# Kernel optimization log

Hardware: AMD Instinct MI355X
Metric: run time of the kernel (lower is better)

## Reference

```python
import jax, jax.numpy as jnp
import numpy as np

N_NODES = 50000
N_EDGES = 800000
L, D_IN, D_HID, D_OUT = 3, 128, 256, 128


def setup_inputs() -> dict:
    key = jax.random.key(0)
    ks = jax.random.split(key, 5)
    x = jax.random.normal(ks[0], (N_NODES, D_IN), dtype=jnp.float32)
    # Kaiming-ish init so activations stay O(1) across 3 stacked layers
    W1 = jax.random.normal(ks[1], (L, D_IN, D_HID), dtype=jnp.float32) / np.sqrt(D_IN)
    b1 = jnp.zeros((L, D_HID), dtype=jnp.float32)
    W2 = jax.random.normal(ks[2], (L, D_HID, D_OUT), dtype=jnp.float32) / np.sqrt(D_HID)
    b2 = jnp.zeros((L, D_OUT), dtype=jnp.float32)
    src = jax.random.randint(ks[3], (N_EDGES,), 0, N_NODES, dtype=jnp.int64)
    dst = jax.random.randint(ks[4], (N_EDGES,), 0, N_NODES, dtype=jnp.int64)
    return {"x": x, "W1": W1, "b1": b1, "W2": W2, "b2": b2, "src": src, "dst": dst}


def reference(x, W1, b1, W2, b2, src, dst):
    # Stacked GIN-style message passing: gather -> scatter-sum -> 2-layer MLP.
    n = x.shape[0]
    for l in range(W1.shape[0]):  # small fixed layer count
        msgs = jnp.take(x, src, axis=0)                     # [E, D] gather
        agg = jax.ops.segment_sum(msgs, dst, num_segments=n)  # [N, D] scatter-add
        h = jax.nn.relu((x + agg) @ W1[l] + b1[l])          # [N, D_hid]
        x = h @ W2[l] + b2[l]                               # [N, D_out]
    return x
```

## Files before the change

### kernel.cpp

```cpp
#include <hip/hip_runtime.h>
#include <hip/hip_bf16.h>
#include <stdint.h>

#define N_NODES 50000
#define N_EDGES 800000
#define D_IN 128
#define D_HID 256
#define D_OUT 128
#define LAYERS 3

typedef __attribute__((ext_vector_type(8))) short bf16x8;
typedef __attribute__((ext_vector_type(4))) float f32x4;
typedef __attribute__((ext_vector_type(4))) unsigned short us4;
typedef __attribute__((ext_vector_type(8))) unsigned short us8;

static __device__ __forceinline__ unsigned short f2bf(float f) {
  union { float f; unsigned int u; } v; v.f = f;
  unsigned int r = v.u + 0x7fff + ((v.u >> 16) & 1);
  return (unsigned short)(r >> 16);
}
static __device__ __forceinline__ float bf2f(unsigned short u) {
  union { unsigned int u; float f; } v; v.u = ((unsigned int)u) << 16;
  return v.f;
}

__global__ __launch_bounds__(256) void hist_kernel(
    const int* __restrict__ dst, int* __restrict__ deg) {
  int e = blockIdx.x * 256 + threadIdx.x;
  if (e < N_EDGES) atomicAdd(&deg[dst[e]], 1);
}

#define SCAN_BLOCKS 196

__global__ __launch_bounds__(256) void scan_a_kernel(
    const int* __restrict__ deg, int* __restrict__ rowptr,
    int* __restrict__ partial) {
  __shared__ int buf[256];
  const int tid = threadIdx.x;
  int gid = blockIdx.x * 256 + tid;
  int v = (gid < N_NODES) ? deg[gid] : 0;
  buf[tid] = v;
  __syncthreads();
  for (int off = 1; off < 256; off <<= 1) {
    int add = (tid >= off) ? buf[tid - off] : 0;
    __syncthreads();
    buf[tid] += add;
    __syncthreads();
  }
  if (gid < N_NODES) rowptr[gid] = buf[tid] - v;
  if (tid == 255) partial[blockIdx.x] = buf[255];
}

__global__ __launch_bounds__(256) void scan_b_kernel(int* __restrict__ partial) {
  __shared__ int buf[256];
  const int tid = threadIdx.x;
  int v = (tid < SCAN_BLOCKS) ? partial[tid] : 0;
  buf[tid] = v;
  __syncthreads();
  for (int off = 1; off < 256; off <<= 1) {
    int add = (tid >= off) ? buf[tid - off] : 0;
    __syncthreads();
    buf[tid] += add;
    __syncthreads();
  }
  if (tid < SCAN_BLOCKS) partial[tid] = buf[tid] - v;
}

__global__ __launch_bounds__(256) void scan_c_kernel(
    int* __restrict__ rowptr, const int* __restrict__ partial,
    int* __restrict__ cursor) {
  int gid = blockIdx.x * 256 + threadIdx.x;
  if (gid < N_NODES) {
    int r = rowptr[gid] + partial[blockIdx.x];
    rowptr[gid] = r;
    cursor[gid] = r;
  }
  if (gid == 0) rowptr[N_NODES] = N_EDGES;
}

__global__ __launch_bounds__(256) void fill_kernel(
    const int* __restrict__ src, const int* __restrict__ dst,
    int* __restrict__ cursor, int* __restrict__ eidx) {
  int e = blockIdx.x * 256 + threadIdx.x;
  if (e >= N_EDGES) return;
  int pos = atomicAdd(&cursor[dst[e]], 1);
  eidx[pos] = src[e];
}

__global__ __launch_bounds__(256) void convert_x(
    const float* __restrict__ x, unsigned short* __restrict__ xb) {
  int i = blockIdx.x * 256 + threadIdx.x;
  if (i >= N_NODES * D_IN / 4) return;
  float4 v = ((const float4*)x)[i];
  us4 p = { f2bf(v.x), f2bf(v.y), f2bf(v.z), f2bf(v.w) };
  ((us4*)xb)[i] = p;
}

__global__ __launch_bounds__(256) void agg_kernel(
    const unsigned short* __restrict__ xb, const int* __restrict__ rowptr,
    const int* __restrict__ eidx, unsigned short* __restrict__ aggb) {
  int n = blockIdx.x * 4 + (threadIdx.x >> 6);
  if (n >= N_NODES) return;
  int t = threadIdx.x & 63;
  const size_t tt = (size_t)t * 2;
  ushort2 own = *(const ushort2*)&xb[(size_t)n * D_IN + tt];
  float a0 = bf2f(own.x), a1 = bf2f(own.y);
  float c0 = 0.f, c1 = 0.f;
  int j = rowptr[n];
  const int end = rowptr[n + 1];
  for (; j + 3 < end; j += 4) {
    int s0 = eidx[j], s1 = eidx[j + 1], s2 = eidx[j + 2], s3 = eidx[j + 3];
    ushort2 v0 = *(const ushort2*)&xb[(size_t)s0 * D_IN + tt];
    ushort2 v1 = *(const ushort2*)&xb[(size_t)s1 * D_IN + tt];
    ushort2 v2 = *(const ushort2*)&xb[(size_t)s2 * D_IN + tt];
    ushort2 v3 = *(const ushort2*)&xb[(size_t)s3 * D_IN + tt];
    a0 += bf2f(v0.x) + bf2f(v1.x);
    a1 += bf2f(v0.y) + bf2f(v1.y);
    c0 += bf2f(v2.x) + bf2f(v3.x);
    c1 += bf2f(v2.y) + bf2f(v3.y);
  }
  for (; j < end; ++j) {
    int s = eidx[j];
    ushort2 v = *(const ushort2*)&xb[(size_t)s * D_IN + tt];
    a0 += bf2f(v.x);
    a1 += bf2f(v.y);
  }
  a0 += c0; a1 += c1;
  ushort2 r = { f2bf(a0), f2bf(a1) };
  *(ushort2*)&aggb[(size_t)n * D_IN + tt] = r;
}

__global__ __launch_bounds__(256) void convert_weights(
    const float* __restrict__ W1, const float* __restrict__ W2,
    unsigned short* __restrict__ w1bf, unsigned short* __restrict__ w2bf) {
  int idx = blockIdx.x * 256 + threadIdx.x;
  const int per = LAYERS * D_IN * D_HID;
  if (idx < per) {
    int l = idx / (D_IN * D_HID);
    int r = idx % (D_IN * D_HID);
    int n = r / D_IN;
    int k = r % D_IN;
    w1bf[idx] = f2bf(W1[(size_t)l * D_IN * D_HID + (size_t)k * D_HID + n]);
  } else {
    int j = idx - per;
    if (j < LAYERS * D_HID * D_OUT) {
      int l = j / (D_HID * D_OUT);
      int r = j % (D_HID * D_OUT);
      int n = r / D_HID;
      int k = r % D_HID;
      w2bf[j] = f2bf(W2[(size_t)l * D_HID * D_OUT + (size_t)k * D_OUT + n]);
    }
  }
}

#define LDA1 136
__global__ __launch_bounds__(256) void mlp1_kernel(
    const unsigned short* __restrict__ aggb, const unsigned short* __restrict__ w1,
    const float* __restrict__ b1, unsigned short* __restrict__ h) {
  __shared__ unsigned short As[64 * LDA1];
  const int tid = threadIdx.x;
  const int block_row = blockIdx.x * 64;

  for (int k = 0; k < 4; ++k) {
    int j = tid + k * 256;
    int row = j >> 4;
    int c8 = j & 15;
    int node = block_row + row;
    if (node >= N_NODES) node = N_NODES - 1;
    us8 v = *(const us8*)&aggb[(size_t)node * D_IN + c8 * 8];
    *(us8*)&As[row * LDA1 + c8 * 8] = v;
  }
  __syncthreads();

  const int wave = tid >> 6;
  const int lane = tid & 63;
  const int lo16 = lane & 15;
  const int hi4  = lane >> 4;
  const int ncol0 = wave * 64;

  f32x4 acc[4][4] = {};
  for (int ks = 0; ks < 4; ++ks) {
    const int koff = ks * 32 + hi4 * 8;
    bf16x8 a[4], b[4];
#pragma unroll
    for (int m = 0; m < 4; ++m)
      a[m] = *(const bf16x8*)&As[(m * 16 + lo16) * LDA1 + koff];
#pragma unroll
    for (int n = 0; n < 4; ++n)
      b[n] = *(const bf16x8*)&w1[(size_t)(ncol0 + n * 16 + lo16) * D_IN + koff];
#pragma unroll
    for (int m = 0; m < 4; ++m)
#pragma unroll
      for (int n = 0; n < 4; ++n)
        acc[m][n] = __builtin_amdgcn_mfma_f32_16x16x32_bf16(a[m], b[n], acc[m][n], 0, 0, 0);
  }

#pragma unroll
  for (int n = 0; n < 4; ++n) {
    int col = ncol0 + n * 16 + lo16;
    float bias = b1[col];
#pragma unroll
    for (int m = 0; m < 4; ++m) {
#pragma unroll
      for (int r = 0; r < 4; ++r) {
        int node = block_row + m * 16 + hi4 * 4 + r;
        if (node < N_NODES) {
          float v = acc[m][n][r] + bias;
          v = v > 0.f ? v : 0.f;
          h[(size_t)node * D_HID + col] = f2bf(v);
        }
      }
    }
  }
}

#define LDA2 264
template <bool FINAL>
__global__ __launch_bounds__(256) void mlp2_kernel(
    const unsigned short* __restrict__ h, const unsigned short* __restrict__ w2,
    const float* __restrict__ b2, float* __restrict__ outf,
    unsigned short* __restrict__ outb) {
  __shared__ unsigned short As[64 * LDA2];
  const int tid = threadIdx.x;
  const int block_row = blockIdx.x * 64;

  for (int k = 0; k < 8; ++k) {
    int j = tid + k * 256;
    int row = j >> 5;
    int c8 = j & 31;
    int node = block_row + row;
    if (node >= N_NODES) node = N_NODES - 1;
    us8 v = *(const us8*)&h[(size_t)node * D_HID + c8 * 8];
    *(us8*)&As[row * LDA2 + c8 * 8] = v;
  }
  __syncthreads();

  const int wave = tid >> 6;
  const int lane = tid & 63;
  const int lo16 = lane & 15;
  const int hi4  = lane >> 4;
  const int ncol0 = wave * 32;

  f32x4 acc[4][2] = {};
  for (int ks = 0; ks < 8; ++ks) {
    const int koff = ks * 32 + hi4 * 8;
    bf16x8 a[4], b[2];
#pragma unroll
    for (int m = 0; m < 4; ++m)
      a[m] = *(const bf16x8*)&As[(m * 16 + lo16) * LDA2 + koff];
#pragma unroll
    for (int n = 0; n < 2; ++n)
      b[n] = *(const bf16x8*)&w2[(size_t)(ncol0 + n * 16 + lo16) * D_HID + koff];
#pragma unroll
    for (int m = 0; m < 4; ++m)
#pragma unroll
      for (int n = 0; n < 2; ++n)
        acc[m][n] = __builtin_amdgcn_mfma_f32_16x16x32_bf16(a[m], b[n], acc[m][n], 0, 0, 0);
  }

#pragma unroll
  for (int n = 0; n < 2; ++n) {
    int col = ncol0 + n * 16 + lo16;
    float bias = b2[col];
#pragma unroll
    for (int m = 0; m < 4; ++m) {
#pragma unroll
      for (int r = 0; r < 4; ++r) {
        int node = block_row + m * 16 + hi4 * 4 + r;
        if (node < N_NODES) {
          float v = acc[m][n][r] + bias;
          if (FINAL) outf[(size_t)node * D_OUT + col] = v;
          else       outb[(size_t)node * D_OUT + col] = f2bf(v);
        }
      }
    }
  }
}

extern "C" void kernel_launch(void* const* d_in, const int* in_sizes, int n_in,
                              void* d_out, int out_size, void* d_ws, size_t ws_size,
                              hipStream_t stream) {
  const float* x0 = (const float*)d_in[0];
  const float* W1 = (const float*)d_in[1];
  const float* b1 = (const float*)d_in[2];
  const float* W2 = (const float*)d_in[3];
  const float* b2 = (const float*)d_in[4];
  const int* src  = (const int*)d_in[5];
  const int* dst  = (const int*)d_in[6];
  float* out = (float*)d_out;

  char* ws = (char*)d_ws;
  size_t off = 0;
  unsigned short* xb   = (unsigned short*)(ws + off); off += (size_t)N_NODES * D_IN * 2;
  unsigned short* aggb = (unsigned short*)(ws + off); off += (size_t)N_NODES * D_IN * 2;
  unsigned short* hbuf = (unsigned short*)(ws + off); off += (size_t)N_NODES * D_HID * 2;
  unsigned short* xbuf = (unsigned short*)(ws + off); off += (size_t)N_NODES * D_OUT * 2;
  unsigned short* w1bf = (unsigned short*)(ws + off); off += (size_t)LAYERS * D_IN * D_HID * 2;
  unsigned short* w2bf = (unsigned short*)(ws + off); off += (size_t)LAYERS * D_HID * D_OUT * 2;
  int* deg     = (int*)(ws + off); off += (size_t)(N_NODES + 1) * 4;
  int* rowptr  = (int*)(ws + off); off += (size_t)(N_NODES + 1) * 4;
  int* cursor  = (int*)(ws + off); off += (size_t)(N_NODES + 1) * 4;
  int* partial = (int*)(ws + off); off += (size_t)SCAN_BLOCKS * 4;
  int* eidx    = (int*)(ws + off); off += (size_t)N_EDGES * 4;

  hipMemsetAsync(deg, 0, (size_t)N_NODES * 4, stream);
  hist_kernel<<<N_EDGES / 256, 256, 0, stream>>>(dst, deg);
  scan_a_kernel<<<SCAN_BLOCKS, 256, 0, stream>>>(deg, rowptr, partial);
  scan_b_kernel<<<1, 256, 0, stream>>>(partial);
  scan_c_kernel<<<SCAN_BLOCKS, 256, 0, stream>>>(rowptr, partial, cursor);
  fill_kernel<<<N_EDGES / 256, 256, 0, stream>>>(src, dst, cursor, eidx);

  convert_x<<<(N_NODES * D_IN / 4 + 255) / 256, 256, 0, stream>>>(x0, xb);
  convert_weights<<<768, 256, 0, stream>>>(W1, W2, w1bf, w2bf);

  const int grid_mlp = (N_NODES + 63) / 64;
  const int grid_agg = (N_NODES + 3) / 4;
  const unsigned short* xcur = xb;
  for (int l = 0; l < LAYERS; ++l) {
    agg_kernel<<<grid_agg, 256, 0, stream>>>(xcur, rowptr, eidx, aggb);
    mlp1_kernel<<<grid_mlp, 256, 0, stream>>>(
        aggb, w1bf + (size_t)l * D_IN * D_HID, b1 + (size_t)l * D_HID, hbuf);
    if (l == LAYERS - 1) {
      mlp2_kernel<true><<<grid_mlp, 256, 0, stream>>>(
          hbuf, w2bf + (size_t)l * D_HID * D_OUT, b2 + (size_t)l * D_OUT, out, nullptr);
    } else {
      mlp2_kernel<false><<<grid_mlp, 256, 0, stream>>>(
          hbuf, w2bf + (size_t)l * D_HID * D_OUT, b2 + (size_t)l * D_OUT, nullptr, xbuf);
    }
    xcur = xbuf;
  }
}
```

Measured before the change: 438.8 us.

## Build CSR via two-level bucket sort with 16-bit edge indices

Replaces the per-node histogram, three-pass scan and per-node atomic fill with a bucketed build. A shared-memory histogram counts edges over 782 buckets of 64 nodes, a single-block scan produces the bucket offsets, and a binning pass writes packed (local dst, src) words into bucket order. A per-bucket kernel then sorts each bucket locally with shared atomics and emits rowptr. Source indices are now stored as 16-bit values, which halves index traffic in the aggregation kernel. The trade-off is heavy global-atomic contention on the 782 bucket cursors, an extra staging buffer, and indices that only fit while the node count stays below 65536.

```diff
diff --git a/kernel.cpp b/kernel.cpp
--- a/kernel.cpp
+++ b/kernel.cpp
@@ -9,6 +9,9 @@
 #define D_OUT 128
 #define LAYERS 3
 
+#define BUCKET_SHIFT 6
+#define NB 782
+
 typedef __attribute__((ext_vector_type(8))) short bf16x8;
 typedef __attribute__((ext_vector_type(4))) float f32x4;
 typedef __attribute__((ext_vector_type(4))) unsigned short us4;
@@ -24,67 +27,89 @@
   return v.f;
 }
 
-__global__ __launch_bounds__(256) void hist_kernel(
-    const int* __restrict__ dst, int* __restrict__ deg) {
-  int e = blockIdx.x * 256 + threadIdx.x;
-  if (e < N_EDGES) atomicAdd(&deg[dst[e]], 1);
-}
-
-#define SCAN_BLOCKS 196
-
-__global__ __launch_bounds__(256) void scan_a_kernel(
-    const int* __restrict__ deg, int* __restrict__ rowptr,
-    int* __restrict__ partial) {
-  __shared__ int buf[256];
+__global__ __launch_bounds__(256) void bhist_kernel(
+    const int* __restrict__ dst, int* __restrict__ bcnt) {
+  __shared__ int h[NB];
+  for (int i = threadIdx.x; i < NB; i += 256) h[i] = 0;
+  __syncthreads();
+  const int base = blockIdx.x * 4096;
+#pragma unroll
+  for (int k = 0; k < 16; ++k) {
+    int e = base + k * 256 + threadIdx.x;
+    if (e < N_EDGES) atomicAdd(&h[dst[e] >> BUCKET_SHIFT], 1);
+  }
+  __syncthreads();
+  for (int i = threadIdx.x; i < NB; i += 256)
+    if (h[i]) atomicAdd(&bcnt[i], h[i]);
+}
+
+__global__ __launch_bounds__(1024) void bscan_kernel(
+    const int* __restrict__ bcnt, int* __restrict__ bbase,
+    int* __restrict__ bcur, int* __restrict__ rowptr) {
+  __shared__ int buf[1024];
   const int tid = threadIdx.x;
-  int gid = blockIdx.x * 256 + tid;
-  int v = (gid < N_NODES) ? deg[gid] : 0;
+  int v = (tid < NB) ? bcnt[tid] : 0;
   buf[tid] = v;
   __syncthreads();
-  for (int off = 1; off < 256; off <<= 1) {
+  for (int off = 1; off < 1024; off <<= 1) {
     int add = (tid >= off) ? buf[tid - off] : 0;
     __syncthreads();
     buf[tid] += add;
     __syncthreads();
   }
-  if (gid < N_NODES) rowptr[gid] = buf[tid] - v;
-  if (tid == 255) partial[blockIdx.x] = buf[255];
-}
-
-__global__ __launch_bounds__(256) void scan_b_kernel(int* __restrict__ partial) {
-  __shared__ int buf[256];
-  const int tid = threadIdx.x;
-  int v = (tid < SCAN_BLOCKS) ? partial[tid] : 0;
-  buf[tid] = v;
-  __syncthreads();
-  for (int off = 1; off < 256; off <<= 1) {
-    int add = (tid >= off) ? buf[tid - off] : 0;
-    __syncthreads();
-    buf[tid] += add;
-    __syncthreads();
-  }
-  if (tid < SCAN_BLOCKS) partial[tid] = buf[tid] - v;
-}
-
-__global__ __launch_bounds__(256) void scan_c_kernel(
-    int* __restrict__ rowptr, const int* __restrict__ partial,
-    int* __restrict__ cursor) {
-  int gid = blockIdx.x * 256 + threadIdx.x;
-  if (gid < N_NODES) {
-    int r = rowptr[gid] + partial[blockIdx.x];
-    rowptr[gid] = r;
-    cursor[gid] = r;
-  }
-  if (gid == 0) rowptr[N_NODES] = N_EDGES;
-}
-
-__global__ __launch_bounds__(256) void fill_kernel(
+  if (tid < NB) {
+    int e0 = buf[tid] - v;
+    bbase[tid] = e0;
+    bcur[tid] = e0;
+  }
+  if (tid == 0) { bbase[NB] = N_EDGES; rowptr[N_NODES] = N_EDGES; }
+}
+
+__global__ __launch_bounds__(256) void bin_kernel(
     const int* __restrict__ src, const int* __restrict__ dst,
-    int* __restrict__ cursor, int* __restrict__ eidx) {
+    int* __restrict__ bcur, unsigned int* __restrict__ staged) {
   int e = blockIdx.x * 256 + threadIdx.x;
   if (e >= N_EDGES) return;
-  int pos = atomicAdd(&cursor[dst[e]], 1);
-  eidx[pos] = src[e];
+  int d = dst[e];
+  int b = d >> BUCKET_SHIFT;
+  int pos = atomicAdd(&bcur[b], 1);
+  staged[pos] = ((unsigned int)(d & 63) << 16) | (unsigned int)src[e];
+}
+
+__global__ __launch_bounds__(256) void bsort_kernel(
+    const unsigned int* __restrict__ staged, const int* __restrict__ bbase,
+    int* __restrict__ rowptr, unsigned short* __restrict__ eidx) {
+  __shared__ int cnt[64];
+  __shared__ int pre[64];
+  __shared__ int cur[64];
+  const int tid = threadIdx.x;
+  const int b = blockIdx.x;
+  const int j0 = bbase[b], j1 = bbase[b + 1];
+  if (tid < 64) cnt[tid] = 0;
+  __syncthreads();
+  for (int j = j0 + tid; j < j1; j += 256)
+    atomicAdd(&cnt[(staged[j] >> 16) & 63], 1);
+  __syncthreads();
+  if (tid < 64) {
+    int c = cnt[tid];
+    int v = c;
+    for (int off = 1; off < 64; off <<= 1) {
+      int n = __shfl_up(v, off);
+      if (tid >= off) v += n;
+    }
+    int ex = v - c;
+    pre[tid] = ex;
+    cur[tid] = ex;
+    int node = (b << BUCKET_SHIFT) + tid;
+    if (node < N_NODES) rowptr[node] = j0 + ex;
+  }
+  __syncthreads();
+  for (int j = j0 + tid; j < j1; j += 256) {
+    unsigned int p = staged[j];
+    int ld = (p >> 16) & 63;
+    int rel = atomicAdd(&cur[ld], 1);
+    eidx[j0 + rel] = (unsigned short)(p & 0xffffu);
+  }
 }
 
 __global__ __launch_bounds__(256) void convert_x(
@@ -98,7 +123,7 @@
 
 __global__ __launch_bounds__(256) void agg_kernel(
     const unsigned short* __restrict__ xb, const int* __restrict__ rowptr,
-    const int* __restrict__ eidx, unsigned short* __restrict__ aggb) {
+    const unsigned short* __restrict__ eidx, unsigned short* __restrict__ aggb) {
   int n = blockIdx.x * 4 + (threadIdx.x >> 6);
   if (n >= N_NODES) return;
   int t = threadIdx.x & 63;
@@ -297,18 +322,18 @@
   unsigned short* xbuf = (unsigned short*)(ws + off); off += (size_t)N_NODES * D_OUT * 2;
   unsigned short* w1bf = (unsigned short*)(ws + off); off += (size_t)LAYERS * D_IN * D_HID * 2;
   unsigned short* w2bf = (unsigned short*)(ws + off); off += (size_t)LAYERS * D_HID * D_OUT * 2;
-  int* deg     = (int*)(ws + off); off += (size_t)(N_NODES + 1) * 4;
-  int* rowptr  = (int*)(ws + off); off += (size_t)(N_NODES + 1) * 4;
-  int* cursor  = (int*)(ws + off); off += (size_t)(N_NODES + 1) * 4;
-  int* partial = (int*)(ws + off); off += (size_t)SCAN_BLOCKS * 4;
-  int* eidx    = (int*)(ws + off); off += (size_t)N_EDGES * 4;
-
-  hipMemsetAsync(deg, 0, (size_t)N_NODES * 4, stream);
-  hist_kernel<<<N_EDGES / 256, 256, 0, stream>>>(dst, deg);
-  scan_a_kernel<<<SCAN_BLOCKS, 256, 0, stream>>>(deg, rowptr, partial);
-  scan_b_kernel<<<1, 256, 0, stream>>>(partial);
-  scan_c_kernel<<<SCAN_BLOCKS, 256, 0, stream>>>(rowptr, partial, cursor);
-  fill_kernel<<<N_EDGES / 256, 256, 0, stream>>>(src, dst, cursor, eidx);
+  int* bcnt   = (int*)(ws + off); off += (size_t)NB * 4;
+  int* bbase  = (int*)(ws + off); off += (size_t)(NB + 1) * 4;
+  int* bcur   = (int*)(ws + off); off += (size_t)NB * 4;
+  int* rowptr = (int*)(ws + off); off += (size_t)(N_NODES + 1) * 4;
+  unsigned int* staged = (unsigned int*)(ws + off); off += (size_t)N_EDGES * 4;
+  unsigned short* eidx = (unsigned short*)(ws + off); off += (size_t)N_EDGES * 2;
+
+  hipMemsetAsync(bcnt, 0, (size_t)NB * 4, stream);
+  bhist_kernel<<<196, 256, 0, stream>>>(dst, bcnt);
+  bscan_kernel<<<1, 1024, 0, stream>>>(bcnt, bbase, bcur, rowptr);
+  bin_kernel<<<N_EDGES / 256, 256, 0, stream>>>(src, dst, bcur, staged);
+  bsort_kernel<<<NB, 256, 0, stream>>>(staged, bbase, rowptr, eidx);
 
   convert_x<<<(N_NODES * D_IN / 4 + 255) / 256, 256, 0, stream>>>(x0, xb);
   convert_weights<<<768, 256, 0, stream>>>(W1, W2, w1bf, w2bf);
```

Measured after the change: 555.1 us. 1.27x slower.
